# Kernel optimization log

Hardware: AMD Instinct MI355X
Metric: run time of the kernel (lower is better)

The kernel has to match this reference:

```python
import jax, jax.numpy as jnp
import numpy as np
import math

B, S, N_EMBD, HEAD_SIZE = 32, 2048, 64, 64

def setup_inputs() -> dict:
    key = jax.random.key(0)
    k1, k2, k3, k4 = jax.random.split(key, 4)
    inputs = jax.random.normal(k1, (B, S, N_EMBD), dtype=jnp.float32)
    # nn.Linear(n_embd, head_size, bias=False) weights: shape (head_size, n_embd)
    scale = 1.0 / math.sqrt(N_EMBD)
    Wq = jax.random.normal(k2, (HEAD_SIZE, N_EMBD), dtype=jnp.float32) * scale
    Wk = jax.random.normal(k3, (HEAD_SIZE, N_EMBD), dtype=jnp.float32) * scale
    Wv = jax.random.normal(k4, (HEAD_SIZE, N_EMBD), dtype=jnp.float32) * scale
    return {"inputs": inputs, "Wq": Wq, "Wk": Wk, "Wv": Wv}

def reference(inputs, Wq, Wk, Wv):
    # q, k, v: [B, S, head_size]
    q = jnp.einsum('bse,he->bsh', inputs, Wq)
    k = jnp.einsum('bse,he->bsh', inputs, Wk)
    v = jnp.einsum('bse,he->bsh', inputs, Wv)
    scores = jnp.einsum('bqh,bkh->bqk', q, k) / jnp.sqrt(jnp.float32(HEAD_SIZE))
    # NOTE: the original torch code calls scores.masked_fill(...) out-of-place
    # and discards the result, so NO causal mask is actually applied.
    attention = jax.nn.softmax(scores, axis=-1)
    out = jnp.einsum('bqk,bkh->bqh', attention, v)  # [B, S, head_size]
    return out
```

## Files before the change

### kernel.cpp

```cpp
#include <hip/hip_runtime.h>


#define BATCH 32
#define SEQ   2048
#define HS    64
#define QSCALE 0.18033688011112042f
#define OTS   72
#define MSTR  68

typedef _Float16 f16x8 __attribute__((ext_vector_type(8)));
typedef _Float16 f16x4 __attribute__((ext_vector_type(4)));
typedef float    f32x4 __attribute__((ext_vector_type(4)));

__global__ __launch_bounds__(256) void prep_w(
    const float* __restrict__ Wq, const float* __restrict__ Wk,
    const float* __restrict__ Wv, _Float16* __restrict__ Wh)
{
    int i = blockIdx.x * 256 + threadIdx.x;
    int rep = i / 12288;
    int j = i - rep * 12288;
    const float* src = (j < 4096) ? Wq : ((j < 8192) ? Wk : Wv);
    float scale = (j < 4096) ? QSCALE : 1.0f;
    Wh[i] = (_Float16)(src[j & 4095] * scale);
}

__global__ __launch_bounds__(256) void proj_kernel(
    const float* __restrict__ x, const _Float16* __restrict__ Wh,
    _Float16* __restrict__ Qh, _Float16* __restrict__ Kh,
    _Float16* __restrict__ Vt)
{
    __shared__ __align__(16) _Float16 ot[64 * OTS];

    const int t    = threadIdx.x;
    const int w    = t >> 6;
    const int lane = t & 63;
    const int lo   = lane & 15;
    const int quad = lane >> 4;
    const long blk0 = (long)blockIdx.x * 64;
    const int  b    = (int)(blk0 / SEQ);
    const int  s0   = (int)(blk0 % SEQ);
    const long rw   = blk0 + w * 16;
    const _Float16* Wrep = Wh + (blockIdx.x & 7) * 12288;

    const float* xp = x + (rw + lo) * HS + quad * 8;
    float4 x0 = *(const float4*)xp;
    float4 x1 = *(const float4*)(xp + 4);
    float4 x2 = *(const float4*)(xp + 32);
    float4 x3 = *(const float4*)(xp + 36);
    f16x8 xb0, xb1;
    xb0[0]=(_Float16)x0.x; xb0[1]=(_Float16)x0.y; xb0[2]=(_Float16)x0.z; xb0[3]=(_Float16)x0.w;
    xb0[4]=(_Float16)x1.x; xb0[5]=(_Float16)x1.y; xb0[6]=(_Float16)x1.z; xb0[7]=(_Float16)x1.w;
    xb1[0]=(_Float16)x2.x; xb1[1]=(_Float16)x2.y; xb1[2]=(_Float16)x2.z; xb1[3]=(_Float16)x2.w;
    xb1[4]=(_Float16)x3.x; xb1[5]=(_Float16)x3.y; xb1[6]=(_Float16)x3.z; xb1[7]=(_Float16)x3.w;

#pragma unroll
    for (int m = 0; m < 3; ++m) {
        const _Float16* Wm = Wrep + m * 4096;
        f32x4 acc[4];
#pragma unroll
        for (int nt = 0; nt < 4; ++nt) { acc[nt][0]=0.f; acc[nt][1]=0.f; acc[nt][2]=0.f; acc[nt][3]=0.f; }
#pragma unroll
        for (int nt = 0; nt < 4; ++nt) {
            f16x8 wa0 = *(const f16x8*)(Wm + (nt * 16 + lo) * 64 + quad * 8);
            f16x8 wa1 = *(const f16x8*)(Wm + (nt * 16 + lo) * 64 + 32 + quad * 8);
            acc[nt] = __builtin_amdgcn_mfma_f32_16x16x32_f16(wa0, xb0, acc[nt], 0, 0, 0);
            acc[nt] = __builtin_amdgcn_mfma_f32_16x16x32_f16(wa1, xb1, acc[nt], 0, 0, 0);
        }
        if (m < 2) {
            _Float16* dst = (m == 0) ? Qh : Kh;
#pragma unroll
            for (int nt = 0; nt < 4; ++nt) {
                f16x4 pk;
                pk[0]=(_Float16)acc[nt][0]; pk[1]=(_Float16)acc[nt][1];
                pk[2]=(_Float16)acc[nt][2]; pk[3]=(_Float16)acc[nt][3];
                *(f16x4*)(dst + (rw + lo) * HS + nt * 16 + quad * 4) = pk;
            }
        } else {
#pragma unroll
            for (int nt = 0; nt < 4; ++nt)
#pragma unroll
                for (int r = 0; r < 4; ++r)
                    ot[(nt * 16 + quad * 4 + r) * OTS + w * 16 + lo] = (_Float16)acc[nt][r];
            __syncthreads();
            const int row = t >> 2, c = t & 3;
            f16x8 r0 = *(const f16x8*)(ot + row * OTS + c * 16);
            f16x8 r1 = *(const f16x8*)(ot + row * OTS + c * 16 + 8);
            _Float16* vd = Vt + ((long)b * HS + row) * SEQ + s0 + c * 16;
            *(f16x8*)vd       = r0;
            *(f16x8*)(vd + 8) = r1;
        }
    }
}

__global__ __launch_bounds__(256) void attn_kernel(
    const _Float16* __restrict__ Q, const _Float16* __restrict__ K,
    const _Float16* __restrict__ Vt, float* __restrict__ out)
{
    __shared__ __align__(16) char smem[35840];
    _Float16* KVb  = (_Float16*)smem;
    float*    obuf = (float*)smem;
    float*    lbuf = obuf + 128 * MSTR;

    const int t    = threadIdx.x;
    const int w    = t >> 6;
    const int lane = t & 63;
    const int lo   = lane & 15;
    const int quad = lane >> 4;
    const int sr   = t >> 2, sc = t & 3;
    const int xr   = lo & 7;

    const int bid = blockIdx.x;
    const int b   = (bid & 7) | ((bid >> 7) << 3);
    const int qt  = (bid >> 3) & 15;
    const int q0  = qt * 128;
    const int qh  = w >> 1;
    const int kh  = w & 1;

    const _Float16* Qb = Q + ((long)b * SEQ + q0 + qh * 64) * HS;
    f16x8 qf[4][2];
#pragma unroll
    for (int q2 = 0; q2 < 4; ++q2) {
        qf[q2][0] = *(const f16x8*)(Qb + (q2 * 16 + lo) * HS + quad * 8);
        qf[q2][1] = *(const f16x8*)(Qb + (q2 * 16 + lo) * HS + 32 + quad * 8);
    }

    const _Float16* Kb = K  + (long)b * SEQ * HS;
    const _Float16* Vb = Vt + (long)b * HS * SEQ;

    const int pr  = (sr & 32) | ((sr & 4) << 2) | ((sr & 24) >> 1) | (sr & 3);
    const int kw0 = pr * 64 + (((2 * sc    ) ^ (pr & 7)) << 3);
    const int kw1 = pr * 64 + (((2 * sc + 1) ^ (pr & 7)) << 3);
    const int vw0 = 4096 + sr * 64 + (((2 * sc    ) ^ (sr & 7)) << 3);
    const int vw1 = 4096 + sr * 64 + (((2 * sc + 1) ^ (sr & 7)) << 3);

    const int kr0 = (kh * 32      + lo) * 64;
    const int kr1 = (kh * 32 + 16 + lo) * 64;
    const int g0  = ((quad    ) ^ xr) << 3;
    const int g1  = ((4 + quad) ^ xr) << 3;
    int voff[4];
#pragma unroll
    for (int ht = 0; ht < 4; ++ht)
        voff[ht] = 4096 + (ht * 16 + lo) * 64 + (((kh * 4 + quad) ^ xr) << 3);

    f32x4 o[4][4], ol[4];
#pragma unroll
    for (int q2 = 0; q2 < 4; ++q2) {
        ol[q2][0]=0.f; ol[q2][1]=0.f; ol[q2][2]=0.f; ol[q2][3]=0.f;
#pragma unroll
        for (int ht = 0; ht < 4; ++ht) { o[q2][ht][0]=0.f; o[q2][ht][1]=0.f; o[q2][ht][2]=0.f; o[q2][ht][3]=0.f; }
    }
    f32x4 zz; zz[0]=0.f; zz[1]=0.f; zz[2]=0.f; zz[3]=0.f;
    f16x8 ones;
#pragma unroll
    for (int j = 0; j < 8; ++j) ones[j] = (_Float16)1.0f;

    const int phase = qt << 1;
    const int key0 = (phase & 31) << 6;
    f16x8 kfA = *(const f16x8*)(Kb + (long)(key0 + sr) * HS + sc * 16);
    f16x8 kfB = *(const f16x8*)(Kb + (long)(key0 + sr) * HS + sc * 16 + 8);
    f16x8 vfA = *(const f16x8*)(Vb + (long)sr * SEQ + key0 + sc * 16);
    f16x8 vfB = *(const f16x8*)(Vb + (long)sr * SEQ + key0 + sc * 16 + 8);

    for (int kt = 0; kt < 32; ++kt) {
        _Float16* Ksp = KVb + (kt & 1) * 8192;
        *(f16x8*)(Ksp + kw0) = kfA;
        *(f16x8*)(Ksp + kw1) = kfB;
        *(f16x8*)(Ksp + vw0) = vfA;
        *(f16x8*)(Ksp + vw1) = vfB;

        const int keyn = ((kt + 1 + phase) & 31) << 6;
        kfA = *(const f16x8*)(Kb + (long)(keyn + sr) * HS + sc * 16);
        kfB = *(const f16x8*)(Kb + (long)(keyn + sr) * HS + sc * 16 + 8);
        vfA = *(const f16x8*)(Vb + (long)sr * SEQ + keyn + sc * 16);
        vfB = *(const f16x8*)(Vb + (long)sr * SEQ + keyn + sc * 16 + 8);

        __syncthreads();

        f16x8 ka00 = *(const f16x8*)(Ksp + kr0 + g0);
        f16x8 ka01 = *(const f16x8*)(Ksp + kr0 + g1);
        f16x8 ka10 = *(const f16x8*)(Ksp + kr1 + g0);
        f16x8 ka11 = *(const f16x8*)(Ksp + kr1 + g1);

        f16x8 vbf[4];
#pragma unroll
        for (int ht = 0; ht < 4; ++ht)
            vbf[ht] = *(const f16x8*)(Ksp + voff[ht]);

#pragma unroll
        for (int q2 = 0; q2 < 4; ++q2) {
            f32x4 s0, s1;
            s0 = __builtin_amdgcn_mfma_f32_16x16x32_f16(ka00, qf[q2][0], zz, 0, 0, 0);
            s0 = __builtin_amdgcn_mfma_f32_16x16x32_f16(ka01, qf[q2][1], s0, 0, 0, 0);
            s1 = __builtin_amdgcn_mfma_f32_16x16x32_f16(ka10, qf[q2][0], zz, 0, 0, 0);
            s1 = __builtin_amdgcn_mfma_f32_16x16x32_f16(ka11, qf[q2][1], s1, 0, 0, 0);

            float e0 = __builtin_amdgcn_exp2f(s0[0]);
            float e1 = __builtin_amdgcn_exp2f(s0[1]);
            float e2 = __builtin_amdgcn_exp2f(s0[2]);
            float e3 = __builtin_amdgcn_exp2f(s0[3]);
            float e4 = __builtin_amdgcn_exp2f(s1[0]);
            float e5 = __builtin_amdgcn_exp2f(s1[1]);
            float e6 = __builtin_amdgcn_exp2f(s1[2]);
            float e7 = __builtin_amdgcn_exp2f(s1[3]);

            f16x8 pa;
            pa[0]=(_Float16)e0; pa[1]=(_Float16)e1; pa[2]=(_Float16)e2; pa[3]=(_Float16)e3;
            pa[4]=(_Float16)e4; pa[5]=(_Float16)e5; pa[6]=(_Float16)e6; pa[7]=(_Float16)e7;

            ol[q2] = __builtin_amdgcn_mfma_f32_16x16x32_f16(pa, ones, ol[q2], 0, 0, 0);
#pragma unroll
            for (int ht = 0; ht < 4; ++ht)
                o[q2][ht] = __builtin_amdgcn_mfma_f32_16x16x32_f16(pa, vbf[ht], o[q2][ht], 0, 0, 0);
        }
    }

    __syncthreads();
    if (kh == 0) {
#pragma unroll
        for (int q2 = 0; q2 < 4; ++q2) {
#pragma unroll
            for (int ht = 0; ht < 4; ++ht)
#pragma unroll
                for (int r = 0; r < 4; ++r)
                    obuf[(qh * 64 + q2 * 16 + quad * 4 + r) * MSTR + ht * 16 + lo] = o[q2][ht][r];
            if (lo == 0) {
#pragma unroll
                for (int r = 0; r < 4; ++r)
                    lbuf[qh * 64 + q2 * 16 + quad * 4 + r] = ol[q2][r];
            }
        }
    }
    __syncthreads();
    if (kh == 1) {
#pragma unroll
        for (int q2 = 0; q2 < 4; ++q2) {
            float linv[4];
#pragma unroll
            for (int r = 0; r < 4; ++r)
                linv[r] = 1.0f / (lbuf[qh * 64 + q2 * 16 + quad * 4 + r] + ol[q2][r]);
#pragma unroll
            for (int ht = 0; ht < 4; ++ht)
#pragma unroll
                for (int r = 0; r < 4; ++r) {
                    const int row = qh * 64 + q2 * 16 + quad * 4 + r;
                    float v = (obuf[row * MSTR + ht * 16 + lo] + o[q2][ht][r]) * linv[r];
                    out[((long)b * SEQ + q0 + row) * HS + ht * 16 + lo] = v;
                }
        }
    }
}

extern "C" void kernel_launch(void* const* d_in, const int* in_sizes, int n_in,
                              void* d_out, int out_size, void* d_ws, size_t ws_size,
                              hipStream_t stream)
{
    const float* x  = (const float*)d_in[0];
    const float* Wq = (const float*)d_in[1];
    const float* Wk = (const float*)d_in[2];
    const float* Wv = (const float*)d_in[3];
    float* out = (float*)d_out;

    const size_t E = (size_t)BATCH * SEQ * HS;
    _Float16* Qh = (_Float16*)d_ws;
    _Float16* Kh = Qh + E;
    _Float16* Vt = Kh + E;
    _Float16* Wh = Vt + E;

    prep_w<<<384, 256, 0, stream>>>(Wq, Wk, Wv, Wh);
    proj_kernel<<<(BATCH * SEQ) / 64, 256, 0, stream>>>(x, Wh, Qh, Kh, Vt);
    attn_kernel<<<BATCH * (SEQ / 128), 256, 0, stream>>>(Qh, Kh, Vt, out);
}
```

Baseline: 136.7 us.

## Process two key tiles per barrier and pack exp results with cvt_pkrtz

```diff
diff --git a/kernel.cpp b/kernel.cpp
--- a/kernel.cpp
+++ b/kernel.cpp
@@ -11,6 +11,7 @@
 typedef _Float16 f16x8 __attribute__((ext_vector_type(8)));
 typedef _Float16 f16x4 __attribute__((ext_vector_type(4)));
 typedef float    f32x4 __attribute__((ext_vector_type(4)));
+typedef unsigned int u32x4 __attribute__((ext_vector_type(4)));
 
 __global__ __launch_bounds__(256) void prep_w(
     const float* __restrict__ Wq, const float* __restrict__ Wk,
@@ -92,11 +93,11 @@
     }
 }
 
-__global__ __launch_bounds__(256) void attn_kernel(
+__global__ __launch_bounds__(256, 2) void attn_kernel(
     const _Float16* __restrict__ Q, const _Float16* __restrict__ K,
     const _Float16* __restrict__ Vt, float* __restrict__ out)
 {
-    __shared__ __align__(16) char smem[35840];
+    __shared__ __align__(16) char smem[65536];
     _Float16* KVb  = (_Float16*)smem;
     float*    obuf = (float*)smem;
     float*    lbuf = obuf + 128 * MSTR;
@@ -156,61 +157,80 @@
 
     const int phase = qt << 1;
     const int key0 = (phase & 31) << 6;
-    f16x8 kfA = *(const f16x8*)(Kb + (long)(key0 + sr) * HS + sc * 16);
-    f16x8 kfB = *(const f16x8*)(Kb + (long)(key0 + sr) * HS + sc * 16 + 8);
-    f16x8 vfA = *(const f16x8*)(Vb + (long)sr * SEQ + key0 + sc * 16);
-    f16x8 vfB = *(const f16x8*)(Vb + (long)sr * SEQ + key0 + sc * 16 + 8);
-
-    for (int kt = 0; kt < 32; ++kt) {
-        _Float16* Ksp = KVb + (kt & 1) * 8192;
-        *(f16x8*)(Ksp + kw0) = kfA;
-        *(f16x8*)(Ksp + kw1) = kfB;
-        *(f16x8*)(Ksp + vw0) = vfA;
-        *(f16x8*)(Ksp + vw1) = vfB;
-
-        const int keyn = ((kt + 1 + phase) & 31) << 6;
-        kfA = *(const f16x8*)(Kb + (long)(keyn + sr) * HS + sc * 16);
-        kfB = *(const f16x8*)(Kb + (long)(keyn + sr) * HS + sc * 16 + 8);
-        vfA = *(const f16x8*)(Vb + (long)sr * SEQ + keyn + sc * 16);
-        vfB = *(const f16x8*)(Vb + (long)sr * SEQ + keyn + sc * 16 + 8);
+    f16x8 kfA0 = *(const f16x8*)(Kb + (long)(key0 + sr) * HS + sc * 16);
+    f16x8 kfB0 = *(const f16x8*)(Kb + (long)(key0 + sr) * HS + sc * 16 + 8);
+    f16x8 vfA0 = *(const f16x8*)(Vb + (long)sr * SEQ + key0 + sc * 16);
+    f16x8 vfB0 = *(const f16x8*)(Vb + (long)sr * SEQ + key0 + sc * 16 + 8);
+    f16x8 kfA1 = *(const f16x8*)(Kb + (long)(key0 + 64 + sr) * HS + sc * 16);
+    f16x8 kfB1 = *(const f16x8*)(Kb + (long)(key0 + 64 + sr) * HS + sc * 16 + 8);
+    f16x8 vfA1 = *(const f16x8*)(Vb + (long)sr * SEQ + key0 + 64 + sc * 16);
+    f16x8 vfB1 = *(const f16x8*)(Vb + (long)sr * SEQ + key0 + 64 + sc * 16 + 8);
+
+    for (int kt2 = 0; kt2 < 16; ++kt2) {
+        _Float16* Bp = KVb + (kt2 & 1) * 16384;
+        *(f16x8*)(Bp + kw0) = kfA0;
+        *(f16x8*)(Bp + kw1) = kfB0;
+        *(f16x8*)(Bp + vw0) = vfA0;
+        *(f16x8*)(Bp + vw1) = vfB0;
+        *(f16x8*)(Bp + 8192 + kw0) = kfA1;
+        *(f16x8*)(Bp + 8192 + kw1) = kfB1;
+        *(f16x8*)(Bp + 8192 + vw0) = vfA1;
+        *(f16x8*)(Bp + 8192 + vw1) = vfB1;
+
+        const int keyn = ((2 * kt2 + 2 + phase) & 31) << 6;
+        kfA0 = *(const f16x8*)(Kb + (long)(keyn + sr) * HS + sc * 16);
+        kfB0 = *(const f16x8*)(Kb + (long)(keyn + sr) * HS + sc * 16 + 8);
+        vfA0 = *(const f16x8*)(Vb + (long)sr * SEQ + keyn + sc * 16);
+        vfB0 = *(const f16x8*)(Vb + (long)sr * SEQ + keyn + sc * 16 + 8);
+        kfA1 = *(const f16x8*)(Kb + (long)(keyn + 64 + sr) * HS + sc * 16);
+        kfB1 = *(const f16x8*)(Kb + (long)(keyn + 64 + sr) * HS + sc * 16 + 8);
+        vfA1 = *(const f16x8*)(Vb + (long)sr * SEQ + keyn + 64 + sc * 16);
+        vfB1 = *(const f16x8*)(Vb + (long)sr * SEQ + keyn + 64 + sc * 16 + 8);
 
         __syncthreads();
 
-        f16x8 ka00 = *(const f16x8*)(Ksp + kr0 + g0);
-        f16x8 ka01 = *(const f16x8*)(Ksp + kr0 + g1);
-        f16x8 ka10 = *(const f16x8*)(Ksp + kr1 + g0);
-        f16x8 ka11 = *(const f16x8*)(Ksp + kr1 + g1);
-
-        f16x8 vbf[4];
-#pragma unroll
-        for (int ht = 0; ht < 4; ++ht)
-            vbf[ht] = *(const f16x8*)(Ksp + voff[ht]);
-
-#pragma unroll
-        for (int q2 = 0; q2 < 4; ++q2) {
-            f32x4 s0, s1;
-            s0 = __builtin_amdgcn_mfma_f32_16x16x32_f16(ka00, qf[q2][0], zz, 0, 0, 0);
-            s0 = __builtin_amdgcn_mfma_f32_16x16x32_f16(ka01, qf[q2][1], s0, 0, 0, 0);
-            s1 = __builtin_amdgcn_mfma_f32_16x16x32_f16(ka10, qf[q2][0], zz, 0, 0, 0);
-            s1 = __builtin_amdgcn_mfma_f32_16x16x32_f16(ka11, qf[q2][1], s1, 0, 0, 0);
-
-            float e0 = __builtin_amdgcn_exp2f(s0[0]);
-            float e1 = __builtin_amdgcn_exp2f(s0[1]);
-            float e2 = __builtin_amdgcn_exp2f(s0[2]);
-            float e3 = __builtin_amdgcn_exp2f(s0[3]);
-            float e4 = __builtin_amdgcn_exp2f(s1[0]);
-            float e5 = __builtin_amdgcn_exp2f(s1[1]);
-            float e6 = __builtin_amdgcn_exp2f(s1[2]);
-            float e7 = __builtin_amdgcn_exp2f(s1[3]);
-
-            f16x8 pa;
-            pa[0]=(_Float16)e0; pa[1]=(_Float16)e1; pa[2]=(_Float16)e2; pa[3]=(_Float16)e3;
-            pa[4]=(_Float16)e4; pa[5]=(_Float16)e5; pa[6]=(_Float16)e6; pa[7]=(_Float16)e7;
-
-            ol[q2] = __builtin_amdgcn_mfma_f32_16x16x32_f16(pa, ones, ol[q2], 0, 0, 0);
+#pragma unroll
+        for (int sub = 0; sub < 2; ++sub) {
+            _Float16* Ksp = Bp + sub * 8192;
+
+            f16x8 ka00 = *(const f16x8*)(Ksp + kr0 + g0);
+            f16x8 ka01 = *(const f16x8*)(Ksp + kr0 + g1);
+            f16x8 ka10 = *(const f16x8*)(Ksp + kr1 + g0);
+            f16x8 ka11 = *(const f16x8*)(Ksp + kr1 + g1);
+
+            f16x8 vbf[4];
 #pragma unroll
             for (int ht = 0; ht < 4; ++ht)
-                o[q2][ht] = __builtin_amdgcn_mfma_f32_16x16x32_f16(pa, vbf[ht], o[q2][ht], 0, 0, 0);
+                vbf[ht] = *(const f16x8*)(Ksp + voff[ht]);
+
+#pragma unroll
+            for (int q2 = 0; q2 < 4; ++q2) {
+                f32x4 s0, s1;
+                s0 = __builtin_amdgcn_mfma_f32_16x16x32_f16(ka00, qf[q2][0], zz, 0, 0, 0);
+                s0 = __builtin_amdgcn_mfma_f32_16x16x32_f16(ka01, qf[q2][1], s0, 0, 0, 0);
+                s1 = __builtin_amdgcn_mfma_f32_16x16x32_f16(ka10, qf[q2][0], zz, 0, 0, 0);
+                s1 = __builtin_amdgcn_mfma_f32_16x16x32_f16(ka11, qf[q2][1], s1, 0, 0, 0);
+
+                u32x4 pw;
+                pw[0] = __builtin_bit_cast(unsigned int,
+                        __builtin_amdgcn_cvt_pkrtz(__builtin_amdgcn_exp2f(s0[0]),
+                                                   __builtin_amdgcn_exp2f(s0[1])));
+                pw[1] = __builtin_bit_cast(unsigned int,
+                        __builtin_amdgcn_cvt_pkrtz(__builtin_amdgcn_exp2f(s0[2]),
+                                                   __builtin_amdgcn_exp2f(s0[3])));
+                pw[2] = __builtin_bit_cast(unsigned int,
+                        __builtin_amdgcn_cvt_pkrtz(__builtin_amdgcn_exp2f(s1[0]),
+                                                   __builtin_amdgcn_exp2f(s1[1])));
+                pw[3] = __builtin_bit_cast(unsigned int,
+                        __builtin_amdgcn_cvt_pkrtz(__builtin_amdgcn_exp2f(s1[2]),
+                                                   __builtin_amdgcn_exp2f(s1[3])));
+                f16x8 pa = __builtin_bit_cast(f16x8, pw);
+
+                ol[q2] = __builtin_amdgcn_mfma_f32_16x16x32_f16(pa, ones, ol[q2], 0, 0, 0);
+#pragma unroll
+                for (int ht = 0; ht < 4; ++ht)
+                    o[q2][ht] = __builtin_amdgcn_mfma_f32_16x16x32_f16(pa, vbf[ht], o[q2][ht], 0, 0, 0);
+            }
         }
     }
 
```

Result: faster. 127.7 us (-6.6%).
